# Kernel optimization log

Hardware: AMD Instinct MI355X
Metric: run time of the kernel (lower is better)

## Reference

```python
import jax, jax.numpy as jnp
import numpy as np

U = 8  # LSTM units

def setup_inputs() -> dict:
    key = jax.random.key(0)
    ks = jax.random.split(key, 6)
    B, T, F = 4096, 512, 32
    x = jax.random.normal(ks[0], (B, T, F), dtype=jnp.float32)
    kernel = jax.random.normal(ks[1], (F, 4 * U), dtype=jnp.float32) * 0.1
    rec_kernel = jax.random.normal(ks[2], (U, 4 * U), dtype=jnp.float32) * 0.1
    bias = jnp.zeros((4 * U,), dtype=jnp.float32)
    w1 = jax.random.normal(ks[3], (U, 64), dtype=jnp.float32) * 0.1
    b1 = jnp.zeros((64,), dtype=jnp.float32)
    w2 = jax.random.normal(ks[4], (64, 4), dtype=jnp.float32) * 0.1
    b2 = jnp.zeros((4,), dtype=jnp.float32)
    return {"x": x, "kernel": kernel, "rec_kernel": rec_kernel, "bias": bias,
            "w1": w1, "b1": b1, "w2": w2, "b2": b2}

def _lstm_last_h(x, kernel, rec_kernel, bias):
    # Precompute input projections for all timesteps in one GEMM: [B,T,4U]
    xz = jnp.einsum('btf,fg->btg', x, kernel) + bias
    B = x.shape[0]
    h0 = jnp.zeros((B, U), dtype=x.dtype)
    c0 = jnp.zeros((B, U), dtype=x.dtype)

    def step(carry, xz_t):
        h, c = carry
        z = xz_t + h @ rec_kernel  # [B,4U]
        i = jax.nn.relu(z[:, 0 * U:1 * U])      # recurrent_activation='relu'
        f = jax.nn.relu(z[:, 1 * U:2 * U])
        g = jnp.tanh(z[:, 2 * U:3 * U])         # activation='tanh'
        o = jax.nn.relu(z[:, 3 * U:4 * U])
        c_new = f * c + i * g
        h_new = o * jnp.tanh(c_new)
        return (h_new, c_new), None

    (h_last, _), _ = jax.lax.scan(step, (h0, c0), jnp.swapaxes(xz, 0, 1))
    return h_last  # [B, U]

def reference(x, kernel, rec_kernel, bias, w1, b1, w2, b2):
    h = _lstm_last_h(x, kernel, rec_kernel, bias)
    h = jax.nn.relu(h @ w1 + b1)
    return jax.nn.sigmoid(h @ w2 + b2)  # [B, 4]
```

## Files before the change

kernel.cpp:

```cpp
#include <hip/hip_runtime.h>
#include <math.h>

#define BATCH   4096
#define TSTEPS  512
#define FDIM    32
#define UNITS   8
#define G4      32
#define CH      8
#define RPB     8

template<int PAT>
__device__ __forceinline__ float swzf(float v) {
    return __int_as_float(__builtin_amdgcn_ds_swizzle(__float_as_int(v), PAT));
}

__device__ __forceinline__ float fast_rcp(float x) { return __builtin_amdgcn_rcpf(x); }

__device__ __forceinline__ float fast_tanh(float x) {
    float e = __expf(2.0f * x);
    return 1.0f - 2.0f * fast_rcp(e + 1.0f);
}

__device__ __forceinline__ float sigmoidf_(float x) {
    return fast_rcp(1.0f + __expf(-x));
}

__global__ __launch_bounds__(256, 2)
void lstm_fused(const float* __restrict__ x,
                const float* __restrict__ kern,
                const float* __restrict__ rk,
                const float* __restrict__ bias,
                const float* __restrict__ w1,
                const float* __restrict__ b1,
                const float* __restrict__ w2,
                const float* __restrict__ b2,
                float* __restrict__ out)
{
    const int tid  = threadIdx.x;
    const int wv   = tid >> 6;
    const int half = (tid >> 5) & 1;
    const int j    = tid & 31;
    const int row  = blockIdx.x * RPB + wv * 2 + half;

    __shared__ __align__(16) float sx[2][4][2][CH * FDIM];

    float Kc[FDIM];
#pragma unroll
    for (int f = 0; f < FDIM; ++f) Kc[f] = kern[f * G4 + j];
    float Rc[UNITS];
#pragma unroll
    for (int u = 0; u < UNITS; ++u) Rc[u] = rk[u * G4 + j];
    const float bj  = bias[j];
    const bool  isg = ((j >> 3) == 2);

    const float* xrow = x + (size_t)row * (TSTEPS * FDIM);

    float h0=0.f,h1=0.f,h2=0.f,h3=0.f,h4=0.f,h5=0.f,h6=0.f,h7=0.f, c=0.f;

    float4 pa, pb;
    {
        const float4* p = (const float4*)xrow;
        float4 a = p[j], b = p[j + 32];
        float4* q = (float4*)&sx[0][wv][half][0];
        q[j] = a; q[j + 32] = b;
        const float4* p1 = (const float4*)(xrow + CH * FDIM);
        pa = p1[j]; pb = p1[j + 32];
    }

    int slot = 0;
    for (int tc = 0; tc < TSTEPS; tc += CH) {
        const float* xt0 = &sx[slot][wv][half][0];
#pragma unroll
        for (int k = 0; k < CH; ++k) {
            const float4* xv4 = (const float4*)(xt0 + k * FDIM);
            float z0 = bj, z1 = 0.f, z2 = 0.f, z3 = 0.f;
#pragma unroll
            for (int f0 = 0; f0 < 8; ++f0) {
                float4 xv = xv4[f0];
                z0 = fmaf(xv.x, Kc[4 * f0 + 0], z0);
                z1 = fmaf(xv.y, Kc[4 * f0 + 1], z1);
                z2 = fmaf(xv.z, Kc[4 * f0 + 2], z2);
                z3 = fmaf(xv.w, Kc[4 * f0 + 3], z3);
            }
            z0 = fmaf(h0, Rc[0], z0); z1 = fmaf(h1, Rc[1], z1);
            z2 = fmaf(h2, Rc[2], z2); z3 = fmaf(h3, Rc[3], z3);
            z0 = fmaf(h4, Rc[4], z0); z1 = fmaf(h5, Rc[5], z1);
            z2 = fmaf(h6, Rc[6], z2); z3 = fmaf(h7, Rc[7], z3);
            float z = (z0 + z1) + (z2 + z3);

            float a = isg ? fast_tanh(z) : fmaxf(z, 0.f);

            float ai = swzf<0x007>(a);
            float af = swzf<0x107>(a);
            float ag = swzf<0x207>(a);
            float ao = swzf<0x307>(a);

            c = fmaf(af, c, ai * ag);
            float hn = ao * fast_tanh(c);

            h0 = swzf<0x018>(hn); h1 = swzf<0x038>(hn);
            h2 = swzf<0x058>(hn); h3 = swzf<0x078>(hn);
            h4 = swzf<0x098>(hn); h5 = swzf<0x0B8>(hn);
            h6 = swzf<0x0D8>(hn); h7 = swzf<0x0F8>(hn);
        }
        if (tc + CH < TSTEPS) {
            float4* q = (float4*)&sx[slot ^ 1][wv][half][0];
            q[j] = pa; q[j + 32] = pb;
            if (tc + 2 * CH < TSTEPS) {
                const float4* p = (const float4*)(xrow + (tc + 2 * CH) * FDIM);
                pa = p[j]; pb = p[j + 32];
            }
            slot ^= 1;
        }
    }

    const float hh[8] = {h0, h1, h2, h3, h4, h5, h6, h7};
    float m0 = b1[j], m1 = b1[j + 32];
#pragma unroll
    for (int u = 0; u < 8; ++u) {
        m0 = fmaf(hh[u], w1[u * 64 + j],      m0);
        m1 = fmaf(hh[u], w1[u * 64 + 32 + j], m1);
    }
    m0 = fmaxf(m0, 0.f);
    m1 = fmaxf(m1, 0.f);

    float p0 = m0 * w2[j * 4 + 0] + m1 * w2[(j + 32) * 4 + 0];
    float p1 = m0 * w2[j * 4 + 1] + m1 * w2[(j + 32) * 4 + 1];
    float p2 = m0 * w2[j * 4 + 2] + m1 * w2[(j + 32) * 4 + 2];
    float p3 = m0 * w2[j * 4 + 3] + m1 * w2[(j + 32) * 4 + 3];

    p0 += swzf<0x041F>(p0); p1 += swzf<0x041F>(p1); p2 += swzf<0x041F>(p2); p3 += swzf<0x041F>(p3);
    p0 += swzf<0x081F>(p0); p1 += swzf<0x081F>(p1); p2 += swzf<0x081F>(p2); p3 += swzf<0x081F>(p3);
    p0 += swzf<0x101F>(p0); p1 += swzf<0x101F>(p1); p2 += swzf<0x101F>(p2); p3 += swzf<0x101F>(p3);
    p0 += swzf<0x201F>(p0); p1 += swzf<0x201F>(p1); p2 += swzf<0x201F>(p2); p3 += swzf<0x201F>(p3);
    p0 += swzf<0x401F>(p0); p1 += swzf<0x401F>(p1); p2 += swzf<0x401F>(p2); p3 += swzf<0x401F>(p3);

    if (j == 0) {
        float4 o;
        o.x = sigmoidf_(p0 + b2[0]);
        o.y = sigmoidf_(p1 + b2[1]);
        o.z = sigmoidf_(p2 + b2[2]);
        o.w = sigmoidf_(p3 + b2[3]);
        *(float4*)&out[row * 4] = o;
    }
}

extern "C" void kernel_launch(void* const* d_in, const int* in_sizes, int n_in,
                              void* d_out, int out_size, void* d_ws, size_t ws_size,
                              hipStream_t stream)
{
    const float* x    = (const float*)d_in[0];
    const float* kern = (const float*)d_in[1];
    const float* rk   = (const float*)d_in[2];
    const float* bias = (const float*)d_in[3];
    const float* w1   = (const float*)d_in[4];
    const float* b1   = (const float*)d_in[5];
    const float* w2   = (const float*)d_in[6];
    const float* b2   = (const float*)d_in[7];

    dim3 grid(BATCH / RPB);
    dim3 block(256);
    lstm_fused<<<grid, block, 0, stream>>>(x, kern, rk, bias, w1, b1, w2, b2, (float*)d_out);
}
```

Baseline: 435.1 us.

## Rewrite LSTM recurrence using bf16 MFMA with 16 rows per wavefront

Replaces the scalar FMA per-gate formulation with bf16 MFMA 16x16x32 instructions that compute input and recurrent projections for 16 batch rows per 64-lane wave. x is loaded directly from global with register double-buffering instead of staging through shared memory, and h is redistributed across lanes via swizzle/permlane swaps. This cuts ALU work per step but introduces bf16 rounding of x, weights and hidden state, and launches only 256 single-wave blocks, which lowers occupancy and latency hiding on the serial recurrence.

```diff
diff --git a/kernel.cpp b/kernel.cpp
--- a/kernel.cpp
+++ b/kernel.cpp
@@ -1,147 +1,165 @@
 #include <hip/hip_runtime.h>
+#include <hip/hip_bf16.h>
 #include <math.h>
 
-#define BATCH   4096
-#define TSTEPS  512
-#define FDIM    32
-#define UNITS   8
-#define G4      32
-#define CH      8
-#define RPB     8
+#define TSTEPS 512
+#define FDIM   32
+
+typedef __attribute__((ext_vector_type(8))) short bf16x8;
+typedef __attribute__((ext_vector_type(4))) float f32x4;
 
 template<int PAT>
 __device__ __forceinline__ float swzf(float v) {
     return __int_as_float(__builtin_amdgcn_ds_swizzle(__float_as_int(v), PAT));
 }
 
+__device__ __forceinline__ float crossf(float v) {
+#if __has_builtin(__builtin_amdgcn_permlane32_swap)
+    unsigned u = __float_as_uint(v);
+    auto r = __builtin_amdgcn_permlane32_swap(u, u, false, false);
+    unsigned c = (r[0] == u) ? r[1] : r[0];
+    return __uint_as_float(c);
+#else
+    return __shfl_xor(v, 32, 64);
+#endif
+}
+
 __device__ __forceinline__ float fast_rcp(float x) { return __builtin_amdgcn_rcpf(x); }
-
 __device__ __forceinline__ float fast_tanh(float x) {
     float e = __expf(2.0f * x);
     return 1.0f - 2.0f * fast_rcp(e + 1.0f);
 }
+__device__ __forceinline__ float sigmoidf_(float x) { return fast_rcp(1.0f + __expf(-x)); }
 
-__device__ __forceinline__ float sigmoidf_(float x) {
-    return fast_rcp(1.0f + __expf(-x));
+__device__ __forceinline__ unsigned short f2bfu(float f) {
+    __hip_bfloat16 h = __float2bfloat16(f);
+    unsigned short u; __builtin_memcpy(&u, &h, 2); return u;
+}
+__device__ __forceinline__ unsigned pk2(float a, float b) {
+    __hip_bfloat162 t = __float22bfloat162_rn(float2{a, b});
+    unsigned w; __builtin_memcpy(&w, &t, 4); return w;
 }
 
-__global__ __launch_bounds__(256, 2)
-void lstm_fused(const float* __restrict__ x,
-                const float* __restrict__ kern,
-                const float* __restrict__ rk,
-                const float* __restrict__ bias,
-                const float* __restrict__ w1,
-                const float* __restrict__ b1,
-                const float* __restrict__ w2,
-                const float* __restrict__ b2,
-                float* __restrict__ out)
+union FR { bf16x8 v; unsigned short u[8]; unsigned w[4]; };
+
+__global__ __launch_bounds__(64)
+void lstm_mfma(const float* __restrict__ x,
+               const float* __restrict__ kern,
+               const float* __restrict__ rk,
+               const float* __restrict__ bias,
+               const float* __restrict__ w1,
+               const float* __restrict__ b1,
+               const float* __restrict__ w2,
+               const float* __restrict__ b2,
+               float* __restrict__ out)
 {
-    const int tid  = threadIdx.x;
-    const int wv   = tid >> 6;
-    const int half = (tid >> 5) & 1;
-    const int j    = tid & 31;
-    const int row  = blockIdx.x * RPB + wv * 2 + half;
+    const int l   = threadIdx.x;
+    const int r15 = l & 15;
+    const int grp = l >> 4;
 
-    __shared__ __align__(16) float sx[2][4][2][CH * FDIM];
+    const int mA = r15 >> 1, bA = r15 & 1;
+    const int kc0 = mA + 8 * bA;
+    const int kc1 = 16 + mA + 8 * bA;
 
-    float Kc[FDIM];
+    FR A0f, A1f, R0f, R1f, hf;
 #pragma unroll
-    for (int f = 0; f < FDIM; ++f) Kc[f] = kern[f * G4 + j];
-    float Rc[UNITS];
-#pragma unroll
-    for (int u = 0; u < UNITS; ++u) Rc[u] = rk[u * G4 + j];
-    const float bj  = bias[j];
-    const bool  isg = ((j >> 3) == 2);
-
-    const float* xrow = x + (size_t)row * (TSTEPS * FDIM);
-
-    float h0=0.f,h1=0.f,h2=0.f,h3=0.f,h4=0.f,h5=0.f,h6=0.f,h7=0.f, c=0.f;
-
-    float4 pa, pb;
-    {
-        const float4* p = (const float4*)xrow;
-        float4 a = p[j], b = p[j + 32];
-        float4* q = (float4*)&sx[0][wv][half][0];
-        q[j] = a; q[j + 32] = b;
-        const float4* p1 = (const float4*)(xrow + CH * FDIM);
-        pa = p1[j]; pb = p1[j + 32];
+    for (int j = 0; j < 8; ++j) {
+        const int f = 8 * grp + j;
+        A0f.u[j] = f2bfu(kern[f * 32 + kc0]);
+        A1f.u[j] = f2bfu(kern[f * 32 + kc1]);
+        R0f.u[j] = (grp == 0) ? f2bfu(rk[j * 32 + kc0]) : (unsigned short)0;
+        R1f.u[j] = (grp == 0) ? f2bfu(rk[j * 32 + kc1]) : (unsigned short)0;
     }
 
-    int slot = 0;
-    for (int tc = 0; tc < TSTEPS; tc += CH) {
-        const float* xt0 = &sx[slot][wv][half][0];
+    f32x4 binit0, binit1;
 #pragma unroll
-        for (int k = 0; k < CH; ++k) {
-            const float4* xv4 = (const float4*)(xt0 + k * FDIM);
-            float z0 = bj, z1 = 0.f, z2 = 0.f, z3 = 0.f;
-#pragma unroll
-            for (int f0 = 0; f0 < 8; ++f0) {
-                float4 xv = xv4[f0];
-                z0 = fmaf(xv.x, Kc[4 * f0 + 0], z0);
-                z1 = fmaf(xv.y, Kc[4 * f0 + 1], z1);
-                z2 = fmaf(xv.z, Kc[4 * f0 + 2], z2);
-                z3 = fmaf(xv.w, Kc[4 * f0 + 3], z3);
-            }
-            z0 = fmaf(h0, Rc[0], z0); z1 = fmaf(h1, Rc[1], z1);
-            z2 = fmaf(h2, Rc[2], z2); z3 = fmaf(h3, Rc[3], z3);
-            z0 = fmaf(h4, Rc[4], z0); z1 = fmaf(h5, Rc[5], z1);
-            z2 = fmaf(h6, Rc[6], z2); z3 = fmaf(h7, Rc[7], z3);
-            float z = (z0 + z1) + (z2 + z3);
-
-            float a = isg ? fast_tanh(z) : fmaxf(z, 0.f);
-
-            float ai = swzf<0x007>(a);
-            float af = swzf<0x107>(a);
-            float ag = swzf<0x207>(a);
-            float ao = swzf<0x307>(a);
-
-            c = fmaf(af, c, ai * ag);
-            float hn = ao * fast_tanh(c);
-
-            h0 = swzf<0x018>(hn); h1 = swzf<0x038>(hn);
-            h2 = swzf<0x058>(hn); h3 = swzf<0x078>(hn);
-            h4 = swzf<0x098>(hn); h5 = swzf<0x0B8>(hn);
-            h6 = swzf<0x0D8>(hn); h7 = swzf<0x0F8>(hn);
-        }
-        if (tc + CH < TSTEPS) {
-            float4* q = (float4*)&sx[slot ^ 1][wv][half][0];
-            q[j] = pa; q[j + 32] = pb;
-            if (tc + 2 * CH < TSTEPS) {
-                const float4* p = (const float4*)(xrow + (tc + 2 * CH) * FDIM);
-                pa = p[j]; pb = p[j + 32];
-            }
-            slot ^= 1;
-        }
+    for (int i = 0; i < 4; ++i) {
+        const int cl = 4 * grp + i, mm = cl >> 1, bb = cl & 1;
+        binit0[i] = bias[mm + 8 * bb];
+        binit1[i] = bias[16 + mm + 8 * bb];
     }
 
-    const float hh[8] = {h0, h1, h2, h3, h4, h5, h6, h7};
-    float m0 = b1[j], m1 = b1[j + 32];
+    hf.w[0] = 0; hf.w[1] = 0; hf.w[2] = 0; hf.w[3] = 0;
+    float cA = 0.f, cB = 0.f;
+    float hv0=0.f,hv1=0.f,hv2=0.f,hv3=0.f,hv4=0.f,hv5=0.f,hv6=0.f,hv7=0.f;
+
+    const size_t row = (size_t)blockIdx.x * 16 + r15;
+    const float* xp = x + row * (TSTEPS * FDIM) + grp * 8;
+
+    auto STEP = [&](const float4& x0, const float4& x1) {
+        FR xf;
+        xf.w[0] = pk2(x0.x, x0.y);
+        xf.w[1] = pk2(x0.z, x0.w);
+        xf.w[2] = pk2(x1.x, x1.y);
+        xf.w[3] = pk2(x1.z, x1.w);
+        f32x4 a0 = __builtin_amdgcn_mfma_f32_16x16x32_bf16(A0f.v, xf.v, binit0, 0, 0, 0);
+        f32x4 a1 = __builtin_amdgcn_mfma_f32_16x16x32_bf16(A1f.v, xf.v, binit1, 0, 0, 0);
+        a0 = __builtin_amdgcn_mfma_f32_16x16x32_bf16(R0f.v, hf.v, a0, 0, 0, 0);
+        a1 = __builtin_amdgcn_mfma_f32_16x16x32_bf16(R1f.v, hf.v, a1, 0, 0, 0);
+        float iA = fmaxf(a0[0], 0.f), fA = fmaxf(a0[1], 0.f);
+        float iB = fmaxf(a0[2], 0.f), fB = fmaxf(a0[3], 0.f);
+        float gA = fast_tanh(a1[0]), oA = fmaxf(a1[1], 0.f);
+        float gB = fast_tanh(a1[2]), oB = fmaxf(a1[3], 0.f);
+        cA = fmaf(fA, cA, iA * gA);
+        cB = fmaf(fB, cB, iB * gB);
+        float hA = oA * fast_tanh(cA);
+        float hB = oB * fast_tanh(cB);
+        float t2 = swzf<0x401F>(hA);
+        float t3 = swzf<0x401F>(hB);
+        float t4 = crossf(hA);
+        float t5 = crossf(hB);
+        float t6 = crossf(t2);
+        float t7 = crossf(t3);
+        hf.w[0] = pk2(hA, hB);
+        hf.w[1] = pk2(t2, t3);
+        hf.w[2] = pk2(t4, t5);
+        hf.w[3] = pk2(t6, t7);
+        hv0 = hA; hv1 = hB; hv2 = t2; hv3 = t3; hv4 = t4; hv5 = t5; hv6 = t6; hv7 = t7;
+    };
+
+#define LD4(t, o) (*(const float4*)(xp + (size_t)(t) * FDIM + (o)))
+    float4 Xa0 = LD4(0, 0), Xa1 = LD4(0, 4);
+    float4 Xb0 = LD4(1, 0), Xb1 = LD4(1, 4);
+
+    for (int t = 0; t < TSTEPS - 2; t += 2) {
+        float4 Na0 = LD4(t + 2, 0), Na1 = LD4(t + 2, 4);
+        float4 Nb0 = LD4(t + 3, 0), Nb1 = LD4(t + 3, 4);
+        STEP(Xa0, Xa1);
+        STEP(Xb0, Xb1);
+        Xa0 = Na0; Xa1 = Na1; Xb0 = Nb0; Xb1 = Nb1;
+    }
+    STEP(Xa0, Xa1);
+    STEP(Xb0, Xb1);
+#undef LD4
+
+    const float hvv[8] = {hv0, hv1, hv2, hv3, hv4, hv5, hv6, hv7};
+    const int g2 = 2 * grp;
+    float o0 = 0.f, o1 = 0.f, o2 = 0.f, o3 = 0.f;
 #pragma unroll
-    for (int u = 0; u < 8; ++u) {
-        m0 = fmaf(hh[u], w1[u * 64 + j],      m0);
-        m1 = fmaf(hh[u], w1[u * 64 + 32 + j], m1);
+    for (int cc = 0; cc < 16; ++cc) {
+        const int col = grp * 16 + cc;
+        float s = b1[col];
+#pragma unroll
+        for (int k = 0; k < 8; ++k)
+            s = fmaf(hvv[k], w1[(k ^ g2) * 64 + col], s);
+        s = fmaxf(s, 0.f);
+        o0 = fmaf(s, w2[col * 4 + 0], o0);
+        o1 = fmaf(s, w2[col * 4 + 1], o1);
+        o2 = fmaf(s, w2[col * 4 + 2], o2);
+        o3 = fmaf(s, w2[col * 4 + 3], o3);
     }
-    m0 = fmaxf(m0, 0.f);
-    m1 = fmaxf(m1, 0.f);
+    o0 += swzf<0x401F>(o0); o1 += swzf<0x401F>(o1);
+    o2 += swzf<0x401F>(o2); o3 += swzf<0x401F>(o3);
+    o0 += crossf(o0); o1 += crossf(o1);
+    o2 += crossf(o2); o3 += crossf(o3);
 
-    float p0 = m0 * w2[j * 4 + 0] + m1 * w2[(j + 32) * 4 + 0];
-    float p1 = m0 * w2[j * 4 + 1] + m1 * w2[(j + 32) * 4 + 1];
-    float p2 = m0 * w2[j * 4 + 2] + m1 * w2[(j + 32) * 4 + 2];
-    float p3 = m0 * w2[j * 4 + 3] + m1 * w2[(j + 32) * 4 + 3];
-
-    p0 += swzf<0x041F>(p0); p1 += swzf<0x041F>(p1); p2 += swzf<0x041F>(p2); p3 += swzf<0x041F>(p3);
-    p0 += swzf<0x081F>(p0); p1 += swzf<0x081F>(p1); p2 += swzf<0x081F>(p2); p3 += swzf<0x081F>(p3);
-    p0 += swzf<0x101F>(p0); p1 += swzf<0x101F>(p1); p2 += swzf<0x101F>(p2); p3 += swzf<0x101F>(p3);
-    p0 += swzf<0x201F>(p0); p1 += swzf<0x201F>(p1); p2 += swzf<0x201F>(p2); p3 += swzf<0x201F>(p3);
-    p0 += swzf<0x401F>(p0); p1 += swzf<0x401F>(p1); p2 += swzf<0x401F>(p2); p3 += swzf<0x401F>(p3);
-
-    if (j == 0) {
-        float4 o;
-        o.x = sigmoidf_(p0 + b2[0]);
-        o.y = sigmoidf_(p1 + b2[1]);
-        o.z = sigmoidf_(p2 + b2[2]);
-        o.w = sigmoidf_(p3 + b2[3]);
-        *(float4*)&out[row * 4] = o;
+    if (l < 16) {
+        float4 r;
+        r.x = sigmoidf_(o0 + b2[0]);
+        r.y = sigmoidf_(o1 + b2[1]);
+        r.z = sigmoidf_(o2 + b2[2]);
+        r.w = sigmoidf_(o3 + b2[3]);
+        *(float4*)&out[((size_t)blockIdx.x * 16 + l) * 4] = r;
     }
 }
 
@@ -158,7 +176,7 @@
     const float* w2   = (const float*)d_in[6];
     const float* b2   = (const float*)d_in[7];
 
-    dim3 grid(BATCH / RPB);
-    dim3 block(256);
-    lstm_fused<<<grid, block, 0, stream>>>(x, kern, rk, bias, w1, b1, w2, b2, (float*)d_out);
+    dim3 grid(4096 / 16);
+    dim3 block(64);
+    lstm_mfma<<<grid, block, 0, stream>>>(x, kern, rk, bias, w1, b1, w2, b2, (float*)d_out);
 }
```

New measurement: 495.5 us. 1.14x slower.
